# Kernel tuning notes

Measured on AMD Instinct MI355X. Metric: run time of the kernel, lower is better.

## Reference

```python
import jax, jax.numpy as jnp
import numpy as np

D_MODEL = 64

def setup_inputs() -> dict:
    key = jax.random.key(0)
    k1, k2, k3, k4, k5, k6 = jax.random.split(key, 6)
    b, h, t, s, d = 2, 8, 384, 384, D_MODEL
    scale = 1.0 / np.sqrt(d)
    return {
        "query": jax.random.normal(k1, (b, h, t, d), dtype=jnp.float32),
        "key": jax.random.normal(k2, (b, h, s, d), dtype=jnp.float32),
        "value": jax.random.normal(k3, (b, h, s, d), dtype=jnp.float32),
        # torch nn.Linear(d,d,bias=False) weight W: y = x @ W.T; store W as (out,in)
        "Wq": jax.random.uniform(k4, (d, d), jnp.float32, -scale, scale),
        "Wk": jax.random.uniform(k5, (d, d), jnp.float32, -scale, scale),
        # v: Linear(d,1) -> weight shape (1,d); store as vector (d,)
        "v_w": jax.random.uniform(k6, (d,), jnp.float32, -scale, scale),
    }

def reference(query, key, value, Wq, Wk, v_w):
    # Linearity lets us project BEFORE broadcasting (same math as projecting
    # the (b,h,t,s,d) expanded tensors, far less FLOPs/memory for the GEMMs).
    qp = jnp.einsum('bhtd,ed->bhte', query, Wq)   # W_q * q
    kp = jnp.einsum('bhsd,ed->bhse', key, Wk)     # W_k * k
    # combined: (b,h,t,s,d) broadcast add + tanh (the big intermediate)
    combined = jnp.tanh(qp[:, :, :, None, :] + kp[:, :, None, :, :])
    score = jnp.einsum('bhtsd,d->bhts', combined, v_w)  # v^T tanh(...)
    attn_weights = jax.nn.softmax(score, axis=-1)        # (b,h,t,s)
    out = jnp.einsum('bhts,bhsd->bhtd', attn_weights, value)
    return (out, attn_weights)
```

## Files before the change

kernel.cpp:

```cpp
#include <hip/hip_runtime.h>
#include <hip/hip_bf16.h>

#define BH 16
#define NT 384
#define NS 384
#define DD 64

static constexpr float TWO_LOG2E = 2.8853900817779268f;
static constexpr float LOG2E     = 1.4426950408889634f;

__device__ float4 g_Ea4[(size_t)BH * NT * DD / 4];
__device__ float4 g_Eb4[(size_t)BH * NS * DD / 4];

__global__ __launch_bounds__(256) void k1_proj(
    const float* __restrict__ q, const float* __restrict__ k,
    const float* __restrict__ Wq, const float* __restrict__ Wk)
{
    __shared__ float xt[32 * 64];
    const int bid    = blockIdx.x;
    const int tensor = bid / 192;
    const int tile   = bid % 192;
    const int tid  = threadIdx.x;
    const int lane = tid & 63;
    const int w    = tid >> 6;

    const float* __restrict__ X = tensor ? k  : q;
    const float* __restrict__ W = tensor ? Wk : Wq;
    float* __restrict__ E = tensor ? (float*)g_Eb4 : (float*)g_Ea4;

    const size_t base = (size_t)tile * 32;

    {
        const float4* __restrict__ src =
            reinterpret_cast<const float4*>(X + base * 64);
        float4* dst = reinterpret_cast<float4*>(xt);
#pragma unroll
        for (int i = 0; i < 2; ++i) dst[tid + i * 256] = src[tid + i * 256];
    }

    float wr[64];
    {
        const float* wrow = W + lane * 64;
#pragma unroll
        for (int i = 0; i < 64; i += 4) {
            float4 v = *reinterpret_cast<const float4*>(wrow + i);
            wr[i] = v.x; wr[i + 1] = v.y; wr[i + 2] = v.z; wr[i + 3] = v.w;
        }
    }
    __syncthreads();

#pragma unroll
    for (int r8 = 0; r8 < 8; ++r8) {
        const int r = w * 8 + r8;
        float a0 = 0.f, a1 = 0.f, a2 = 0.f, a3 = 0.f;
#pragma unroll
        for (int d4 = 0; d4 < 16; ++d4) {
            const float4 xv = *reinterpret_cast<const float4*>(&xt[r * 64 + d4 * 4]);
            a0 = fmaf(xv.x, wr[d4 * 4 + 0], a0);
            a1 = fmaf(xv.y, wr[d4 * 4 + 1], a1);
            a2 = fmaf(xv.z, wr[d4 * 4 + 2], a2);
            a3 = fmaf(xv.w, wr[d4 * 4 + 3], a3);
        }
        const float dot = (a0 + a1) + (a2 + a3);
        E[(base + r) * 64 + lane] = __builtin_amdgcn_exp2f(TWO_LOG2E * dot);
    }
}

__global__ __launch_bounds__(256) void k2_fused(
    const float* __restrict__ v_w, const float* __restrict__ V,
    float* __restrict__ out, float* __restrict__ attn)
{
    __shared__ float stage[64 * 68];

    const int bid  = blockIdx.x;
    const int bh   = bid / 48;
    const int t0   = (bid % 48) * 8;
    const int tid  = threadIdx.x;
    const int lane = tid & 63;
    const int wv   = __builtin_amdgcn_readfirstlane(tid >> 6);
    const int r0   = t0 + 2 * wv;

    float C0 = 0.f;
#pragma unroll
    for (int i = 0; i < 64; ++i) C0 += v_w[i];

    const float* __restrict__ ea0 = (const float*)g_Ea4 + ((size_t)bh * NT + r0) * 64;
    const float* __restrict__ ea1 = ea0 + 64;
    const float* __restrict__ Eb  = (const float*)g_Eb4 + (size_t)bh * NS * 64;

    float p0[6], p1[6];

    for (int sc = 0; sc < 6; ++sc) {
        __syncthreads();
        {
            const float4* __restrict__ src =
                reinterpret_cast<const float4*>(Eb + (size_t)sc * 64 * 64);
#pragma unroll
            for (int i = 0; i < 4; ++i) {
                const int j = tid + i * 256;
                const float4 v = src[j];
                const int s  = j >> 4;
                const int e4 = j & 15;
                stage[(e4 * 4 + 0) * 65 + s] = v.x;
                stage[(e4 * 4 + 1) * 65 + s] = v.y;
                stage[(e4 * 4 + 2) * 65 + s] = v.z;
                stage[(e4 * 4 + 3) * 65 + s] = v.w;
            }
        }
        __syncthreads();

        float a00 = 0.f, a01 = 0.f, a02 = 0.f, a03 = 0.f;
        float a10 = 0.f, a11 = 0.f, a12 = 0.f, a13 = 0.f;
#pragma unroll
        for (int e = 0; e < 64; e += 4) {
            const float b0 = stage[(e + 0) * 65 + lane];
            const float b1 = stage[(e + 1) * 65 + lane];
            const float b2 = stage[(e + 2) * 65 + lane];
            const float b3 = stage[(e + 3) * 65 + lane];
            a00 = fmaf(v_w[e + 0], __builtin_amdgcn_rcpf(fmaf(ea0[e + 0], b0, 1.f)), a00);
            a01 = fmaf(v_w[e + 1], __builtin_amdgcn_rcpf(fmaf(ea0[e + 1], b1, 1.f)), a01);
            a02 = fmaf(v_w[e + 2], __builtin_amdgcn_rcpf(fmaf(ea0[e + 2], b2, 1.f)), a02);
            a03 = fmaf(v_w[e + 3], __builtin_amdgcn_rcpf(fmaf(ea0[e + 3], b3, 1.f)), a03);
            a10 = fmaf(v_w[e + 0], __builtin_amdgcn_rcpf(fmaf(ea1[e + 0], b0, 1.f)), a10);
            a11 = fmaf(v_w[e + 1], __builtin_amdgcn_rcpf(fmaf(ea1[e + 1], b1, 1.f)), a11);
            a12 = fmaf(v_w[e + 2], __builtin_amdgcn_rcpf(fmaf(ea1[e + 2], b2, 1.f)), a12);
            a13 = fmaf(v_w[e + 3], __builtin_amdgcn_rcpf(fmaf(ea1[e + 3], b3, 1.f)), a13);
        }
        p0[sc] = C0 - 2.f * ((a00 + a01) + (a02 + a03));
        p1[sc] = C0 - 2.f * ((a10 + a11) + (a12 + a13));
    }

    {
        float m0 = fmaxf(fmaxf(fmaxf(p0[0], p0[1]), fmaxf(p0[2], p0[3])), fmaxf(p0[4], p0[5]));
        float m1 = fmaxf(fmaxf(fmaxf(p1[0], p1[1]), fmaxf(p1[2], p1[3])), fmaxf(p1[4], p1[5]));
#pragma unroll
        for (int o = 32; o > 0; o >>= 1) {
            m0 = fmaxf(m0, __shfl_xor(m0, o, 64));
            m1 = fmaxf(m1, __shfl_xor(m1, o, 64));
        }
        float s0 = 0.f, s1 = 0.f;
#pragma unroll
        for (int i = 0; i < 6; ++i) {
            p0[i] = __builtin_amdgcn_exp2f((p0[i] - m0) * LOG2E);
            p1[i] = __builtin_amdgcn_exp2f((p1[i] - m1) * LOG2E);
            s0 += p0[i];
            s1 += p1[i];
        }
#pragma unroll
        for (int o = 32; o > 0; o >>= 1) {
            s0 += __shfl_xor(s0, o, 64);
            s1 += __shfl_xor(s1, o, 64);
        }
        const float i0 = __builtin_amdgcn_rcpf(s0);
        const float i1 = __builtin_amdgcn_rcpf(s1);
        float* __restrict__ ar0 = attn + ((size_t)bh * NT + r0) * NS;
        float* __restrict__ ar1 = ar0 + NS;
#pragma unroll
        for (int i = 0; i < 6; ++i) {
            p0[i] *= i0;
            p1[i] *= i1;
            ar0[i * 64 + lane] = p0[i];
            ar1[i * 64 + lane] = p1[i];
        }
    }

    const int g  = lane >> 4;
    const int d4 = (lane & 15) * 4;
    float4 O0 = {0.f, 0.f, 0.f, 0.f};
    float4 O1 = {0.f, 0.f, 0.f, 0.f};
    const float4* __restrict__ Vg =
        reinterpret_cast<const float4*>(V + (size_t)bh * NS * 64);

    for (int sc = 0; sc < 6; ++sc) {
        __syncthreads();
        {
#pragma unroll
            for (int i = 0; i < 4; ++i) {
                const int j = tid + i * 256;
                const float4 v = Vg[(size_t)sc * 1024 + j];
                const int row = j >> 4;
                const int c4  = j & 15;
                *reinterpret_cast<float4*>(&stage[row * 68 + c4 * 4]) = v;
            }
        }
        __syncthreads();

#pragma unroll
        for (int s4 = 0; s4 < 16; ++s4) {
            const int sl = s4 * 4 + g;
            const float4 v4 = *reinterpret_cast<const float4*>(&stage[sl * 68 + d4]);
            const float q0 = __shfl(p0[sc], sl, 64);
            const float q1 = __shfl(p1[sc], sl, 64);
            O0.x = fmaf(q0, v4.x, O0.x); O0.y = fmaf(q0, v4.y, O0.y);
            O0.z = fmaf(q0, v4.z, O0.z); O0.w = fmaf(q0, v4.w, O0.w);
            O1.x = fmaf(q1, v4.x, O1.x); O1.y = fmaf(q1, v4.y, O1.y);
            O1.z = fmaf(q1, v4.z, O1.z); O1.w = fmaf(q1, v4.w, O1.w);
        }
    }

#pragma unroll
    for (int o = 16; o <= 32; o <<= 1) {
        O0.x += __shfl_xor(O0.x, o, 64); O0.y += __shfl_xor(O0.y, o, 64);
        O0.z += __shfl_xor(O0.z, o, 64); O0.w += __shfl_xor(O0.w, o, 64);
        O1.x += __shfl_xor(O1.x, o, 64); O1.y += __shfl_xor(O1.y, o, 64);
        O1.z += __shfl_xor(O1.z, o, 64); O1.w += __shfl_xor(O1.w, o, 64);
    }
    if (g == 0) {
        float* __restrict__ op = out + ((size_t)bh * NT + r0) * 64 + d4;
        *reinterpret_cast<float4*>(op)      = O0;
        *reinterpret_cast<float4*>(op + 64) = O1;
    }
}

extern "C" void kernel_launch(void* const* d_in, const int* in_sizes, int n_in,
                              void* d_out, int out_size, void* d_ws, size_t ws_size,
                              hipStream_t stream) {
    const float* q  = (const float*)d_in[0];
    const float* k  = (const float*)d_in[1];
    const float* v  = (const float*)d_in[2];
    const float* Wq = (const float*)d_in[3];
    const float* Wk = (const float*)d_in[4];
    const float* vw = (const float*)d_in[5];

    float* out  = (float*)d_out;
    float* attn = out + (size_t)BH * NT * DD;

    k1_proj <<<384, 256, 0, stream>>>(q, k, Wq, Wk);
    k2_fused<<<768, 256, 0, stream>>>(vw, v, out, attn);
}
```

Baseline: 122.7 us.

## Keep key projections in registers per wave and widen blocks to twelve query rows

Each of six waves now holds its 64 key rows of exp(2·Wk k) in registers. Each block processes 12 query rows, whose Ea values are wave-uniform loads. This removes the per-chunk LDS transpose staging of Eb and its LDS reads in the score loop, and it reuses each Eb load across more query rows. The softmax drops the max subtraction, which relies on the score being bounded by the sum of |v_w|. Probabilities and block-wide sums now go through shared memory instead of wave shuffles. The costs are higher register pressure (64-float arrays at 384 threads) and an uneven V staging loop.

Result: slower. 137.6 us (+12.1%).

```diff
diff --git a/kernel.cpp b/kernel.cpp
--- a/kernel.cpp
+++ b/kernel.cpp
@@ -66,106 +66,78 @@
     }
 }
 
-__global__ __launch_bounds__(256) void k2_fused(
+__global__ __launch_bounds__(384, 3) void k2_fused(
     const float* __restrict__ v_w, const float* __restrict__ V,
     float* __restrict__ out, float* __restrict__ attn)
 {
-    __shared__ float stage[64 * 68];
+    __shared__ float Pl[12 * 388];
+    __shared__ float Vt[64 * 68];
+    __shared__ float ssum[12 * 8];
 
     const int bid  = blockIdx.x;
-    const int bh   = bid / 48;
-    const int t0   = (bid % 48) * 8;
+    const int bh   = bid >> 5;
+    const int t0   = (bid & 31) * 12;
     const int tid  = threadIdx.x;
     const int lane = tid & 63;
     const int wv   = __builtin_amdgcn_readfirstlane(tid >> 6);
-    const int r0   = t0 + 2 * wv;
 
     float C0 = 0.f;
 #pragma unroll
     for (int i = 0; i < 64; ++i) C0 += v_w[i];
 
-    const float* __restrict__ ea0 = (const float*)g_Ea4 + ((size_t)bh * NT + r0) * 64;
-    const float* __restrict__ ea1 = ea0 + 64;
-    const float* __restrict__ Eb  = (const float*)g_Eb4 + (size_t)bh * NS * 64;
-
-    float p0[6], p1[6];
-
-    for (int sc = 0; sc < 6; ++sc) {
-        __syncthreads();
-        {
-            const float4* __restrict__ src =
-                reinterpret_cast<const float4*>(Eb + (size_t)sc * 64 * 64);
-#pragma unroll
-            for (int i = 0; i < 4; ++i) {
-                const int j = tid + i * 256;
-                const float4 v = src[j];
-                const int s  = j >> 4;
-                const int e4 = j & 15;
-                stage[(e4 * 4 + 0) * 65 + s] = v.x;
-                stage[(e4 * 4 + 1) * 65 + s] = v.y;
-                stage[(e4 * 4 + 2) * 65 + s] = v.z;
-                stage[(e4 * 4 + 3) * 65 + s] = v.w;
-            }
-        }
-        __syncthreads();
-
-        float a00 = 0.f, a01 = 0.f, a02 = 0.f, a03 = 0.f;
-        float a10 = 0.f, a11 = 0.f, a12 = 0.f, a13 = 0.f;
+    float eb[64];
+    {
+        const float* __restrict__ ebp =
+            (const float*)g_Eb4 + ((size_t)bh * NS + wv * 64 + lane) * 64;
+#pragma unroll
+        for (int i = 0; i < 16; ++i) {
+            const float4 v = *reinterpret_cast<const float4*>(ebp + i * 4);
+            eb[i * 4 + 0] = v.x; eb[i * 4 + 1] = v.y;
+            eb[i * 4 + 2] = v.z; eb[i * 4 + 3] = v.w;
+        }
+    }
+
+    const float* __restrict__ ea =
+        (const float*)g_Ea4 + ((size_t)bh * NT + t0) * 64;
+
+    float p[12];
+#pragma unroll
+    for (int r = 0; r < 12; ++r) {
+        const float* __restrict__ ear = ea + r * 64;
+        float a0 = 0.f, a1 = 0.f, a2 = 0.f, a3 = 0.f;
 #pragma unroll
         for (int e = 0; e < 64; e += 4) {
-            const float b0 = stage[(e + 0) * 65 + lane];
-            const float b1 = stage[(e + 1) * 65 + lane];
-            const float b2 = stage[(e + 2) * 65 + lane];
-            const float b3 = stage[(e + 3) * 65 + lane];
-            a00 = fmaf(v_w[e + 0], __builtin_amdgcn_rcpf(fmaf(ea0[e + 0], b0, 1.f)), a00);
-            a01 = fmaf(v_w[e + 1], __builtin_amdgcn_rcpf(fmaf(ea0[e + 1], b1, 1.f)), a01);
-            a02 = fmaf(v_w[e + 2], __builtin_amdgcn_rcpf(fmaf(ea0[e + 2], b2, 1.f)), a02);
-            a03 = fmaf(v_w[e + 3], __builtin_amdgcn_rcpf(fmaf(ea0[e + 3], b3, 1.f)), a03);
-            a10 = fmaf(v_w[e + 0], __builtin_amdgcn_rcpf(fmaf(ea1[e + 0], b0, 1.f)), a10);
-            a11 = fmaf(v_w[e + 1], __builtin_amdgcn_rcpf(fmaf(ea1[e + 1], b1, 1.f)), a11);
-            a12 = fmaf(v_w[e + 2], __builtin_amdgcn_rcpf(fmaf(ea1[e + 2], b2, 1.f)), a12);
-            a13 = fmaf(v_w[e + 3], __builtin_amdgcn_rcpf(fmaf(ea1[e + 3], b3, 1.f)), a13);
-        }
-        p0[sc] = C0 - 2.f * ((a00 + a01) + (a02 + a03));
-        p1[sc] = C0 - 2.f * ((a10 + a11) + (a12 + a13));
-    }
-
-    {
-        float m0 = fmaxf(fmaxf(fmaxf(p0[0], p0[1]), fmaxf(p0[2], p0[3])), fmaxf(p0[4], p0[5]));
-        float m1 = fmaxf(fmaxf(fmaxf(p1[0], p1[1]), fmaxf(p1[2], p1[3])), fmaxf(p1[4], p1[5]));
-#pragma unroll
-        for (int o = 32; o > 0; o >>= 1) {
-            m0 = fmaxf(m0, __shfl_xor(m0, o, 64));
-            m1 = fmaxf(m1, __shfl_xor(m1, o, 64));
-        }
-        float s0 = 0.f, s1 = 0.f;
-#pragma unroll
-        for (int i = 0; i < 6; ++i) {
-            p0[i] = __builtin_amdgcn_exp2f((p0[i] - m0) * LOG2E);
-            p1[i] = __builtin_amdgcn_exp2f((p1[i] - m1) * LOG2E);
-            s0 += p0[i];
-            s1 += p1[i];
-        }
-#pragma unroll
-        for (int o = 32; o > 0; o >>= 1) {
-            s0 += __shfl_xor(s0, o, 64);
-            s1 += __shfl_xor(s1, o, 64);
-        }
-        const float i0 = __builtin_amdgcn_rcpf(s0);
-        const float i1 = __builtin_amdgcn_rcpf(s1);
-        float* __restrict__ ar0 = attn + ((size_t)bh * NT + r0) * NS;
-        float* __restrict__ ar1 = ar0 + NS;
-#pragma unroll
-        for (int i = 0; i < 6; ++i) {
-            p0[i] *= i0;
-            p1[i] *= i1;
-            ar0[i * 64 + lane] = p0[i];
-            ar1[i * 64 + lane] = p1[i];
-        }
+            a0 = fmaf(v_w[e + 0], __builtin_amdgcn_rcpf(fmaf(ear[e + 0], eb[e + 0], 1.f)), a0);
+            a1 = fmaf(v_w[e + 1], __builtin_amdgcn_rcpf(fmaf(ear[e + 1], eb[e + 1], 1.f)), a1);
+            a2 = fmaf(v_w[e + 2], __builtin_amdgcn_rcpf(fmaf(ear[e + 2], eb[e + 2], 1.f)), a2);
+            a3 = fmaf(v_w[e + 3], __builtin_amdgcn_rcpf(fmaf(ear[e + 3], eb[e + 3], 1.f)), a3);
+        }
+        p[r] = C0 - 2.f * ((a0 + a1) + (a2 + a3));
+    }
+
+#pragma unroll
+    for (int r = 0; r < 12; ++r) {
+        p[r] = __builtin_amdgcn_exp2f(p[r] * LOG2E);
+        float s = p[r];
+#pragma unroll
+        for (int o = 32; o > 0; o >>= 1) s += __shfl_xor(s, o, 64);
+        if (lane == 0) ssum[r * 8 + wv] = s;
+    }
+    __syncthreads();
+
+#pragma unroll
+    for (int r = 0; r < 12; ++r) {
+        const float tot = ((ssum[r * 8 + 0] + ssum[r * 8 + 1]) +
+                           (ssum[r * 8 + 2] + ssum[r * 8 + 3])) +
+                          (ssum[r * 8 + 4] + ssum[r * 8 + 5]);
+        p[r] *= __builtin_amdgcn_rcpf(tot);
+        Pl[r * 388 + wv * 64 + lane] = p[r];
+        attn[((size_t)bh * NT + t0 + r) * NS + wv * 64 + lane] = p[r];
     }
 
     const int g  = lane >> 4;
-    const int d4 = (lane & 15) * 4;
+    const int dq = (lane & 15) * 4;
+    const int r0 = 2 * wv, r1 = 2 * wv + 1;
     float4 O0 = {0.f, 0.f, 0.f, 0.f};
     float4 O1 = {0.f, 0.f, 0.f, 0.f};
     const float4* __restrict__ Vg =
@@ -173,24 +145,22 @@
 
     for (int sc = 0; sc < 6; ++sc) {
         __syncthreads();
-        {
-#pragma unroll
-            for (int i = 0; i < 4; ++i) {
-                const int j = tid + i * 256;
-                const float4 v = Vg[(size_t)sc * 1024 + j];
-                const int row = j >> 4;
-                const int c4  = j & 15;
-                *reinterpret_cast<float4*>(&stage[row * 68 + c4 * 4]) = v;
-            }
+        for (int j = tid; j < 1024; j += 384) {
+            const float4 v = Vg[sc * 1024 + j];
+            const int row = j >> 4;
+            const int c4  = j & 15;
+            *reinterpret_cast<float4*>(&Vt[row * 68 + c4 * 4]) = v;
         }
         __syncthreads();
 
+        const float* __restrict__ P0 = &Pl[r0 * 388 + sc * 64];
+        const float* __restrict__ P1 = &Pl[r1 * 388 + sc * 64];
 #pragma unroll
         for (int s4 = 0; s4 < 16; ++s4) {
             const int sl = s4 * 4 + g;
-            const float4 v4 = *reinterpret_cast<const float4*>(&stage[sl * 68 + d4]);
-            const float q0 = __shfl(p0[sc], sl, 64);
-            const float q1 = __shfl(p1[sc], sl, 64);
+            const float4 v4 = *reinterpret_cast<const float4*>(&Vt[sl * 68 + dq]);
+            const float q0 = P0[sl];
+            const float q1 = P1[sl];
             O0.x = fmaf(q0, v4.x, O0.x); O0.y = fmaf(q0, v4.y, O0.y);
             O0.z = fmaf(q0, v4.z, O0.z); O0.w = fmaf(q0, v4.w, O0.w);
             O1.x = fmaf(q1, v4.x, O1.x); O1.y = fmaf(q1, v4.y, O1.y);
@@ -206,7 +176,7 @@
         O1.z += __shfl_xor(O1.z, o, 64); O1.w += __shfl_xor(O1.w, o, 64);
     }
     if (g == 0) {
-        float* __restrict__ op = out + ((size_t)bh * NT + r0) * 64 + d4;
+        float* __restrict__ op = out + ((size_t)bh * NT + t0 + r0) * 64 + dq;
         *reinterpret_cast<float4*>(op)      = O0;
         *reinterpret_cast<float4*>(op + 64) = O1;
     }
@@ -226,5 +196,5 @@
     float* attn = out + (size_t)BH * NT * DD;
 
     k1_proj <<<384, 256, 0, stream>>>(q, k, Wq, Wk);
-    k2_fused<<<768, 256, 0, stream>>>(vw, v, out, attn);
+    k2_fused<<<512, 384, 0, stream>>>(vw, v, out, attn);
 }
```
